# Kernel tuning notes

Measured on AMD Instinct MI355X. Metric: run time of the kernel, lower is better.

Reference implementation:

```python
import jax, jax.numpy as jnp
import numpy as np

N = 50000   # nodes
E = 800000  # edges (avg degree 16)
F = 64      # num_node_features
H = 64      # hidden_channels
C = 2       # num_classes
G = 32      # graphs in batch


def gcn_conv(x, src, dst, ew, W, b):
    """PyG GCNConv: h = x @ W; add self-loops (weight 1); symmetric norm
    D^{-1/2} (A+I) D^{-1/2}; scatter-add messages to dst; add bias."""
    n = x.shape[0]
    loop = jnp.arange(n)
    s = jnp.concatenate([src, loop])
    d = jnp.concatenate([dst, loop])
    w = jnp.concatenate([ew, jnp.ones((n,), x.dtype)])
    deg = jax.ops.segment_sum(w, d, num_segments=n)
    dis = jnp.where(deg > 0, jax.lax.rsqrt(deg), 0.0)
    norm = dis[s] * w * dis[d]                      # [E+N]
    h = x @ W                                       # [n, H]
    out = jax.ops.segment_sum(h[s] * norm[:, None], d, num_segments=n)
    return out + b


def setup_inputs() -> dict:
    key = jax.random.key(0)
    ks = jax.random.split(key, 12)
    glorot = lambda k, fi, fo: jax.random.normal(k, (fi, fo), jnp.float32) * np.float32(1.0 / np.sqrt(fi))
    return {
        "x": jax.random.normal(ks[0], (N, F), jnp.float32),
        "edge_index": jax.random.randint(ks[1], (2, E), 0, N),
        "edge_attr": jax.random.uniform(ks[2], (E,), jnp.float32),
        "batch": jnp.sort(jax.random.randint(ks[3], (N,), 0, G)),
        "W1": glorot(ks[4], F, H), "b1": jnp.zeros((H,), jnp.float32),
        "W2": glorot(ks[5], H, H), "b2": jnp.zeros((H,), jnp.float32),
        "W3": glorot(ks[6], H, H), "b3": jnp.zeros((H,), jnp.float32),
        "Wl": glorot(ks[7], H, C), "bl": jnp.zeros((C,), jnp.float32),
    }


def reference(x, edge_index, edge_attr, batch, W1, b1, W2, b2, W3, b3, Wl, bl):
    src, dst = edge_index[0], edge_index[1]
    h = jax.nn.relu(gcn_conv(x, src, dst, edge_attr, W1, b1))
    h = jax.nn.relu(gcn_conv(h, src, dst, edge_attr, W2, b2))
    h = gcn_conv(h, src, dst, edge_attr, W3, b3)
    # global_mean_pool over batch ids
    sums = jax.ops.segment_sum(h, batch, num_segments=G)
    cnt = jax.ops.segment_sum(jnp.ones((h.shape[0],), h.dtype), batch, num_segments=G)
    pooled = sums / jnp.maximum(cnt, 1.0)[:, None]
    # dropout treated as identity (eval mode) for deterministic reference
    return pooled @ Wl + bl
```

## Files before the change

kernel.cpp:

```cpp
#include <hip/hip_runtime.h>


#define FEAT 64
#define NGRAPH 32
#define SCAN_BLK 512
#define POOL_SPAN 64

__device__ __forceinline__ float4 fma4(float s, float4 v, float4 a) {
    a.x = fmaf(s, v.x, a.x); a.y = fmaf(s, v.y, a.y);
    a.z = fmaf(s, v.z, a.z); a.w = fmaf(s, v.w, a.w);
    return a;
}


__global__ void k_cnt(const int* __restrict__ dst, int* __restrict__ cnt,
                      int* __restrict__ rank, int e) {
    int i = blockIdx.x * blockDim.x + threadIdx.x;
    int stride = gridDim.x * blockDim.x;
    for (; i < e; i += stride) rank[i] = atomicAdd(&cnt[dst[i]], 1);
}

__global__ void k_scan_block(const int* __restrict__ cnt, int n,
                             int* __restrict__ row_ptr, int* __restrict__ part) {
    __shared__ int s[SCAN_BLK];
    int tid = threadIdx.x;
    int i = blockIdx.x * SCAN_BLK + tid;
    int v = (i < n) ? cnt[i] : 0;
    s[tid] = v;
    __syncthreads();
    for (int o = 1; o < SCAN_BLK; o <<= 1) {
        int t = (tid >= o) ? s[tid - o] : 0;
        __syncthreads();
        s[tid] += t;
        __syncthreads();
    }
    if (i < n) row_ptr[i] = s[tid] - v;
    if (tid == SCAN_BLK - 1) part[blockIdx.x] = s[tid];
}

__global__ void k_scan_top(int* __restrict__ part, int nb) {
    __shared__ int s[SCAN_BLK];
    int tid = threadIdx.x;
    int v = (tid < nb) ? part[tid] : 0;
    s[tid] = v;
    __syncthreads();
    for (int o = 1; o < SCAN_BLK; o <<= 1) {
        int t = (tid >= o) ? s[tid - o] : 0;
        __syncthreads();
        s[tid] += t;
        __syncthreads();
    }
    if (tid < nb) part[tid] = s[tid] - v;
}

__global__ void k_scan_add(int* __restrict__ row_ptr, const int* __restrict__ part,
                           int n, int e) {
    int i = blockIdx.x * blockDim.x + threadIdx.x;
    if (i < n) row_ptr[i] += part[i >> 9];
    if (i == 0) row_ptr[n] = e;
}

__global__ void k_fill(const int* __restrict__ src, const int* __restrict__ dst,
                       const float* __restrict__ ew, const int* __restrict__ rank,
                       const int* __restrict__ row_ptr, int2* __restrict__ csr, int e) {
    int i = blockIdx.x * blockDim.x + threadIdx.x;
    int stride = gridDim.x * blockDim.x;
    for (; i < e; i += stride) {
        int pos = row_ptr[dst[i]] + rank[i];
        csr[pos] = make_int2(src[i], __float_as_int(ew[i]));
    }
}

__global__ void k_degdis(const int* __restrict__ row_ptr, const int2* __restrict__ csr,
                         float* __restrict__ dis, int n) {
    int i = blockIdx.x * blockDim.x + threadIdx.x;
    if (i >= n) return;
    int beg = row_ptr[i], end = row_ptr[i + 1];
    float deg = 1.0f;
    for (int j = beg; j < end; ++j) deg += __int_as_float(csr[j].y);
    dis[i] = rsqrtf(deg);
}

__global__ void k_norm(const int* __restrict__ row_ptr, int2* __restrict__ csr,
                       const float* __restrict__ dis, int n) {
    int i = blockIdx.x * blockDim.x + threadIdx.x;
    if (i >= n) return;
    int beg = row_ptr[i], end = row_ptr[i + 1];
    float dd = dis[i];
    for (int j = beg; j < end; ++j) {
        int2 e = csr[j];
        float nm = dis[e.x] * __int_as_float(e.y) * dd;
        csr[j] = make_int2(e.x, __float_as_int(nm));
    }
}


__global__ void k_gemm(const float4* __restrict__ X4, const float* __restrict__ W,
                       float4* __restrict__ H4, int n) {
    __shared__ float4 w4[FEAT][16];
    int tid = threadIdx.x;
    for (int t = tid; t < FEAT * 16; t += 256) {
        int k = t >> 4, j4 = t & 15;
        w4[k][j4] = ((const float4*)W)[k * 16 + j4];
    }
    __syncthreads();
    int j4 = tid & 15;
    int r  = tid >> 4;
    int i  = blockIdx.x * 16 + r;
    if (i >= n) return;
    const float4* xr = X4 + (size_t)i * 16;
    float4 a0 = make_float4(0.f, 0.f, 0.f, 0.f);
    float4 a1 = make_float4(0.f, 0.f, 0.f, 0.f);
    #pragma unroll
    for (int kk = 0; kk < 16; ++kk) {
        float4 xv = xr[kk];
        int k = kk * 4;
        float4 w0 = w4[k + 0][j4];
        float4 w1 = w4[k + 1][j4];
        float4 w2 = w4[k + 2][j4];
        float4 w3 = w4[k + 3][j4];
        a0 = fma4(xv.x, w0, a0);
        a1 = fma4(xv.y, w1, a1);
        a0 = fma4(xv.z, w2, a0);
        a1 = fma4(xv.w, w3, a1);
    }
    float4 r4;
    r4.x = a0.x + a1.x; r4.y = a0.y + a1.y;
    r4.z = a0.z + a1.z; r4.w = a0.w + a1.w;
    H4[(size_t)i * 16 + j4] = r4;
}

__global__ void k_conv(const float4* __restrict__ H4, const int* __restrict__ row_ptr,
                       const int2* __restrict__ csr, const float* __restrict__ dis,
                       const float4* __restrict__ bias4, float4* __restrict__ OUT4,
                       int n, int do_relu) {
    int t = blockIdx.x * blockDim.x + threadIdx.x;
    int node = t >> 3;
    int sub = t & 7;
    if (node >= n) return;
    int beg = row_ptr[node];
    int end = row_ptr[node + 1];
    float4 a0 = make_float4(0.f, 0.f, 0.f, 0.f);
    float4 a1 = make_float4(0.f, 0.f, 0.f, 0.f);
    float4 c0 = make_float4(0.f, 0.f, 0.f, 0.f);
    float4 c1 = make_float4(0.f, 0.f, 0.f, 0.f);
    int j = beg;
    for (; j + 2 <= end; j += 2) {
        int2 e0 = csr[j];
        int2 e1 = csr[j + 1];
        float n0 = __int_as_float(e0.y);
        float n1 = __int_as_float(e1.y);
        float4 h00 = H4[e0.x * 16 + sub];
        float4 h01 = H4[e0.x * 16 + 8 + sub];
        float4 h10 = H4[e1.x * 16 + sub];
        float4 h11 = H4[e1.x * 16 + 8 + sub];
        a0 = fma4(n0, h00, a0);
        a1 = fma4(n0, h01, a1);
        c0 = fma4(n1, h10, c0);
        c1 = fma4(n1, h11, c1);
    }
    if (j < end) {
        int2 e0 = csr[j];
        float n0 = __int_as_float(e0.y);
        a0 = fma4(n0, H4[e0.x * 16 + sub], a0);
        a1 = fma4(n0, H4[e0.x * 16 + 8 + sub], a1);
    }
    float di = dis[node];
    float d2 = di * di;
    float4 s0 = H4[node * 16 + sub];
    float4 s1 = H4[node * 16 + 8 + sub];
    float4 bl0 = bias4[sub];
    float4 bl1 = bias4[8 + sub];
    float4 r0, r1;
    r0.x = a0.x + c0.x; r0.y = a0.y + c0.y; r0.z = a0.z + c0.z; r0.w = a0.w + c0.w;
    r1.x = a1.x + c1.x; r1.y = a1.y + c1.y; r1.z = a1.z + c1.z; r1.w = a1.w + c1.w;
    r0 = fma4(d2, s0, r0);
    r1 = fma4(d2, s1, r1);
    r0.x += bl0.x; r0.y += bl0.y; r0.z += bl0.z; r0.w += bl0.w;
    r1.x += bl1.x; r1.y += bl1.y; r1.z += bl1.z; r1.w += bl1.w;
    if (do_relu) {
        r0.x = fmaxf(r0.x, 0.f); r0.y = fmaxf(r0.y, 0.f);
        r0.z = fmaxf(r0.z, 0.f); r0.w = fmaxf(r0.w, 0.f);
        r1.x = fmaxf(r1.x, 0.f); r1.y = fmaxf(r1.y, 0.f);
        r1.z = fmaxf(r1.z, 0.f); r1.w = fmaxf(r1.w, 0.f);
    }
    OUT4[node * 16 + sub] = r0;
    OUT4[node * 16 + 8 + sub] = r1;
}


__global__ void k_pool(const float* __restrict__ H, const int* __restrict__ batch,
                       float* __restrict__ sums, int n) {
    int wid = (blockIdx.x * blockDim.x + threadIdx.x) >> 6;
    int lane = threadIdx.x & 63;
    int beg = wid * POOL_SPAN;
    if (beg >= n) return;
    int end = min(beg + POOL_SPAN, n);
    float acc = 0.f;
    int cur = batch[beg];
    for (int i = beg; i < end; ++i) {
        int g = batch[i];
        if (g != cur) {
            atomicAdd(&sums[cur * FEAT + lane], acc);
            acc = 0.f;
            cur = g;
        }
        acc += H[(size_t)i * FEAT + lane];
    }
    atomicAdd(&sums[cur * FEAT + lane], acc);
}

__device__ __forceinline__ int lb(const int* __restrict__ a, int n, int v) {
    int lo = 0, hi = n;
    while (lo < hi) { int m = (lo + hi) >> 1; if (a[m] < v) lo = m + 1; else hi = m; }
    return lo;
}

__global__ void k_head(const float* __restrict__ sums, const int* __restrict__ batch,
                       int n, const float* __restrict__ Wl, const float* __restrict__ bl,
                       float* __restrict__ out, int C) {
    int t = threadIdx.x;
    if (t >= NGRAPH * C) return;
    int g = t / C, c = t % C;
    int start = lb(batch, n, g);
    int end = lb(batch, n, g + 1);
    float inv = 1.0f / fmaxf((float)(end - start), 1.0f);
    float acc = bl[c];
    #pragma unroll
    for (int f = 0; f < FEAT; ++f)
        acc = fmaf(sums[g * FEAT + f] * inv, Wl[f * C + c], acc);
    out[g * C + c] = acc;
}


extern "C" void kernel_launch(void* const* d_in, const int* in_sizes, int n_in,
                              void* d_out, int out_size, void* d_ws, size_t ws_size,
                              hipStream_t stream) {
    const float* x     = (const float*)d_in[0];
    const int*   ei    = (const int*)d_in[1];
    const float* ew    = (const float*)d_in[2];
    const int*   batch = (const int*)d_in[3];
    const float* W1 = (const float*)d_in[4];
    const float* b1 = (const float*)d_in[5];
    const float* W2 = (const float*)d_in[6];
    const float* b2 = (const float*)d_in[7];
    const float* W3 = (const float*)d_in[8];
    const float* b3 = (const float*)d_in[9];
    const float* Wl = (const float*)d_in[10];
    const float* bl = (const float*)d_in[11];
    float* out = (float*)d_out;

    const int N = in_sizes[3];
    const int E = in_sizes[2];
    const int C = in_sizes[11];

    const int* src = ei;
    const int* dst = ei + E;

    size_t need = 0;
    auto sz = [&](size_t bytes) { need += (bytes + 255) & ~(size_t)255; };
    sz((size_t)N * 4); sz((size_t)N * 4); sz((size_t)(N + 1) * 4);
    sz((size_t)E * 4); sz((size_t)SCAN_BLK * 4);
    sz((size_t)E * 8);
    sz((size_t)N * FEAT * 4); sz((size_t)N * FEAT * 4);
    sz((size_t)NGRAPH * FEAT * 4);
    if (need > ws_size) return;

    char* p = (char*)d_ws;
    auto carve = [&](size_t bytes) {
        char* r = p;
        p += (bytes + 255) & ~(size_t)255;
        return r;
    };
    float* dis      = (float*)carve((size_t)N * 4);
    int*   cnt      = (int*)  carve((size_t)N * 4);
    int*   row_ptr  = (int*)  carve((size_t)(N + 1) * 4);
    int*   rank     = (int*)  carve((size_t)E * 4);
    int*   part     = (int*)  carve((size_t)SCAN_BLK * 4);
    int2*  csr      = (int2*) carve((size_t)E * 8);
    float* bufA     = (float*)carve((size_t)N * FEAT * 4);
    float* bufB     = (float*)carve((size_t)N * FEAT * 4);
    float* sums     = (float*)carve((size_t)NGRAPH * FEAT * 4);

    const int blkN  = (N + 255) / 256;
    const int blkE  = (E + 255) / 256;
    const int nScan = (N + SCAN_BLK - 1) / SCAN_BLK;
    const int blkC  = (N * 8 + 255) / 256;
    const int blkG  = (N + 15) / 16;
    const int blkP  = (N + 4 * POOL_SPAN - 1) / (4 * POOL_SPAN);

    hipMemsetAsync(cnt, 0, (size_t)N * 4, stream);
    hipMemsetAsync(sums, 0, (size_t)NGRAPH * FEAT * 4, stream);

    k_cnt<<<blkE, 256, 0, stream>>>(dst, cnt, rank, E);
    k_scan_block<<<nScan, SCAN_BLK, 0, stream>>>(cnt, N, row_ptr, part);
    k_scan_top<<<1, SCAN_BLK, 0, stream>>>(part, nScan);
    k_scan_add<<<blkN, 256, 0, stream>>>(row_ptr, part, N, E);
    k_fill<<<blkE, 256, 0, stream>>>(src, dst, ew, rank, row_ptr, csr, E);
    k_degdis<<<blkN, 256, 0, stream>>>(row_ptr, csr, dis, N);
    k_norm<<<blkN, 256, 0, stream>>>(row_ptr, csr, dis, N);

    k_gemm<<<blkG, 256, 0, stream>>>((const float4*)x, W1, (float4*)bufA, N);
    k_conv<<<blkC, 256, 0, stream>>>((const float4*)bufA, row_ptr, csr, dis,
                                     (const float4*)b1, (float4*)bufB, N, 1);
    k_gemm<<<blkG, 256, 0, stream>>>((const float4*)bufB, W2, (float4*)bufA, N);
    k_conv<<<blkC, 256, 0, stream>>>((const float4*)bufA, row_ptr, csr, dis,
                                     (const float4*)b2, (float4*)bufB, N, 1);
    k_gemm<<<blkG, 256, 0, stream>>>((const float4*)bufB, W3, (float4*)bufA, N);
    k_conv<<<blkC, 256, 0, stream>>>((const float4*)bufA, row_ptr, csr, dis,
                                     (const float4*)b3, (float4*)bufB, N, 0);

    k_pool<<<blkP, 256, 0, stream>>>(bufB, batch, sums, N);
    k_head<<<1, 64, 0, stream>>>(sums, batch, N, Wl, bl, out, C);
}
```

Measured before the change: 326.8 us.

## Fuse GCN aggregation with the next layer's dense transform

Adds a k_convgemm kernel that gathers neighbor features, applies norm, bias and ReLU, stages the resulting 32 rows in shared memory, and then multiplies them by the next layer's weight matrix in the same block. It replaces the conv+gemm pairs for layers 1→2 and 2→3, removing two full N×64 intermediate writes and reads and two launches. In exchange, the block pays for the weight load and a barrier, shared memory use per block grows, and the GEMM phase must wait for the slowest gather row in the block. Some loads are also inlined directly into fma calls with no semantic change.

New measurement: 317.3 us. 2.9% less time.

```diff
diff --git a/kernel.cpp b/kernel.cpp
--- a/kernel.cpp
+++ b/kernel.cpp
@@ -115,14 +115,10 @@
     for (int kk = 0; kk < 16; ++kk) {
         float4 xv = xr[kk];
         int k = kk * 4;
-        float4 w0 = w4[k + 0][j4];
-        float4 w1 = w4[k + 1][j4];
-        float4 w2 = w4[k + 2][j4];
-        float4 w3 = w4[k + 3][j4];
-        a0 = fma4(xv.x, w0, a0);
-        a1 = fma4(xv.y, w1, a1);
-        a0 = fma4(xv.z, w2, a0);
-        a1 = fma4(xv.w, w3, a1);
+        a0 = fma4(xv.x, w4[k + 0][j4], a0);
+        a1 = fma4(xv.y, w4[k + 1][j4], a1);
+        a0 = fma4(xv.z, w4[k + 2][j4], a0);
+        a1 = fma4(xv.w, w4[k + 3][j4], a1);
     }
     float4 r4;
     r4.x = a0.x + a1.x; r4.y = a0.y + a1.y;
@@ -150,14 +146,10 @@
         int2 e1 = csr[j + 1];
         float n0 = __int_as_float(e0.y);
         float n1 = __int_as_float(e1.y);
-        float4 h00 = H4[e0.x * 16 + sub];
-        float4 h01 = H4[e0.x * 16 + 8 + sub];
-        float4 h10 = H4[e1.x * 16 + sub];
-        float4 h11 = H4[e1.x * 16 + 8 + sub];
-        a0 = fma4(n0, h00, a0);
-        a1 = fma4(n0, h01, a1);
-        c0 = fma4(n1, h10, c0);
-        c1 = fma4(n1, h11, c1);
+        a0 = fma4(n0, H4[e0.x * 16 + sub], a0);
+        a1 = fma4(n0, H4[e0.x * 16 + 8 + sub], a1);
+        c0 = fma4(n1, H4[e1.x * 16 + sub], c0);
+        c1 = fma4(n1, H4[e1.x * 16 + 8 + sub], c1);
     }
     if (j < end) {
         int2 e0 = csr[j];
@@ -167,15 +159,13 @@
     }
     float di = dis[node];
     float d2 = di * di;
-    float4 s0 = H4[node * 16 + sub];
-    float4 s1 = H4[node * 16 + 8 + sub];
-    float4 bl0 = bias4[sub];
-    float4 bl1 = bias4[8 + sub];
     float4 r0, r1;
     r0.x = a0.x + c0.x; r0.y = a0.y + c0.y; r0.z = a0.z + c0.z; r0.w = a0.w + c0.w;
     r1.x = a1.x + c1.x; r1.y = a1.y + c1.y; r1.z = a1.z + c1.z; r1.w = a1.w + c1.w;
-    r0 = fma4(d2, s0, r0);
-    r1 = fma4(d2, s1, r1);
+    r0 = fma4(d2, H4[node * 16 + sub], r0);
+    r1 = fma4(d2, H4[node * 16 + 8 + sub], r1);
+    float4 bl0 = bias4[sub];
+    float4 bl1 = bias4[8 + sub];
     r0.x += bl0.x; r0.y += bl0.y; r0.z += bl0.z; r0.w += bl0.w;
     r1.x += bl1.x; r1.y += bl1.y; r1.z += bl1.z; r1.w += bl1.w;
     if (do_relu) {
@@ -186,6 +176,91 @@
     }
     OUT4[node * 16 + sub] = r0;
     OUT4[node * 16 + 8 + sub] = r1;
+}
+
+__global__ void k_convgemm(const float4* __restrict__ H4, const int* __restrict__ row_ptr,
+                           const int2* __restrict__ csr, const float* __restrict__ dis,
+                           const float4* __restrict__ bias4, const float* __restrict__ Wn,
+                           float4* __restrict__ OUT4, int n) {
+    __shared__ float4 w4[FEAT][16];
+    __shared__ float4 hrow[32][17];
+    int tid = threadIdx.x;
+    for (int t = tid; t < FEAT * 16; t += 256) {
+        int k = t >> 4, j4 = t & 15;
+        w4[k][j4] = ((const float4*)Wn)[k * 16 + j4];
+    }
+
+    int lr   = tid >> 3;
+    int sub  = tid & 7;
+    int node = blockIdx.x * 32 + lr;
+    bool valid = node < n;
+    if (valid) {
+        int beg = row_ptr[node];
+        int end = row_ptr[node + 1];
+        float4 a0 = make_float4(0.f, 0.f, 0.f, 0.f);
+        float4 a1 = make_float4(0.f, 0.f, 0.f, 0.f);
+        float4 c0 = make_float4(0.f, 0.f, 0.f, 0.f);
+        float4 c1 = make_float4(0.f, 0.f, 0.f, 0.f);
+        int j = beg;
+        for (; j + 2 <= end; j += 2) {
+            int2 e0 = csr[j];
+            int2 e1 = csr[j + 1];
+            float n0 = __int_as_float(e0.y);
+            float n1 = __int_as_float(e1.y);
+            a0 = fma4(n0, H4[e0.x * 16 + sub], a0);
+            a1 = fma4(n0, H4[e0.x * 16 + 8 + sub], a1);
+            c0 = fma4(n1, H4[e1.x * 16 + sub], c0);
+            c1 = fma4(n1, H4[e1.x * 16 + 8 + sub], c1);
+        }
+        if (j < end) {
+            int2 e0 = csr[j];
+            float n0 = __int_as_float(e0.y);
+            a0 = fma4(n0, H4[e0.x * 16 + sub], a0);
+            a1 = fma4(n0, H4[e0.x * 16 + 8 + sub], a1);
+        }
+        float di = dis[node];
+        float d2 = di * di;
+        float4 r0, r1;
+        r0.x = a0.x + c0.x; r0.y = a0.y + c0.y; r0.z = a0.z + c0.z; r0.w = a0.w + c0.w;
+        r1.x = a1.x + c1.x; r1.y = a1.y + c1.y; r1.z = a1.z + c1.z; r1.w = a1.w + c1.w;
+        r0 = fma4(d2, H4[node * 16 + sub], r0);
+        r1 = fma4(d2, H4[node * 16 + 8 + sub], r1);
+        float4 bl0 = bias4[sub];
+        float4 bl1 = bias4[8 + sub];
+        r0.x = fmaxf(r0.x + bl0.x, 0.f); r0.y = fmaxf(r0.y + bl0.y, 0.f);
+        r0.z = fmaxf(r0.z + bl0.z, 0.f); r0.w = fmaxf(r0.w + bl0.w, 0.f);
+        r1.x = fmaxf(r1.x + bl1.x, 0.f); r1.y = fmaxf(r1.y + bl1.y, 0.f);
+        r1.z = fmaxf(r1.z + bl1.z, 0.f); r1.w = fmaxf(r1.w + bl1.w, 0.f);
+        hrow[lr][sub] = r0;
+        hrow[lr][8 + sub] = r1;
+    }
+    __syncthreads();
+
+    int j4 = tid & 15;
+    int rr = tid >> 4;
+    #pragma unroll
+    for (int half = 0; half < 2; ++half) {
+        int lrow = rr + half * 16;
+        int grow = blockIdx.x * 32 + lrow;
+        if (grow < n) {
+            const float4* xr = hrow[lrow];
+            float4 a0 = make_float4(0.f, 0.f, 0.f, 0.f);
+            float4 a1 = make_float4(0.f, 0.f, 0.f, 0.f);
+            #pragma unroll
+            for (int kk = 0; kk < 16; ++kk) {
+                float4 xv = xr[kk];
+                int k = kk * 4;
+                a0 = fma4(xv.x, w4[k + 0][j4], a0);
+                a1 = fma4(xv.y, w4[k + 1][j4], a1);
+                a0 = fma4(xv.z, w4[k + 2][j4], a0);
+                a1 = fma4(xv.w, w4[k + 3][j4], a1);
+            }
+            float4 r4;
+            r4.x = a0.x + a1.x; r4.y = a0.y + a1.y;
+            r4.z = a0.z + a1.z; r4.w = a0.w + a1.w;
+            OUT4[(size_t)grow * 16 + j4] = r4;
+        }
+    }
 }
 
 
@@ -286,6 +361,7 @@
     const int blkE  = (E + 255) / 256;
     const int nScan = (N + SCAN_BLK - 1) / SCAN_BLK;
     const int blkC  = (N * 8 + 255) / 256;
+    const int blkF  = (N + 31) / 32;
     const int blkG  = (N + 15) / 16;
     const int blkP  = (N + 4 * POOL_SPAN - 1) / (4 * POOL_SPAN);
 
@@ -301,12 +377,10 @@
     k_norm<<<blkN, 256, 0, stream>>>(row_ptr, csr, dis, N);
 
     k_gemm<<<blkG, 256, 0, stream>>>((const float4*)x, W1, (float4*)bufA, N);
-    k_conv<<<blkC, 256, 0, stream>>>((const float4*)bufA, row_ptr, csr, dis,
-                                     (const float4*)b1, (float4*)bufB, N, 1);
-    k_gemm<<<blkG, 256, 0, stream>>>((const float4*)bufB, W2, (float4*)bufA, N);
-    k_conv<<<blkC, 256, 0, stream>>>((const float4*)bufA, row_ptr, csr, dis,
-                                     (const float4*)b2, (float4*)bufB, N, 1);
-    k_gemm<<<blkG, 256, 0, stream>>>((const float4*)bufB, W3, (float4*)bufA, N);
+    k_convgemm<<<blkF, 256, 0, stream>>>((const float4*)bufA, row_ptr, csr, dis,
+                                         (const float4*)b1, W2, (float4*)bufB, N);
+    k_convgemm<<<blkF, 256, 0, stream>>>((const float4*)bufB, row_ptr, csr, dis,
+                                         (const float4*)b2, W3, (float4*)bufA, N);
     k_conv<<<blkC, 256, 0, stream>>>((const float4*)bufA, row_ptr, csr, dis,
                                      (const float4*)b3, (float4*)bufB, N, 0);
 
```
